# Kernel optimization log

Measured on AMD Instinct MI355X. Metric: run time of the kernel, lower is better.

## Reference

```python
import jax, jax.numpy as jnp
import numpy as np

T, H, F, E, TOP_K = 2048, 1024, 4096, 8, 2


def setup_inputs() -> dict:
    key = jax.random.key(0)
    k0, k1, k2, k3, k4 = jax.random.split(key, 5)
    return {
        "hidden_states": jax.random.normal(k0, (T, H), dtype=jnp.float32),
        "gate_w": jax.random.normal(k1, (E, H), dtype=jnp.float32) * 0.02,  # [E, H] (out, in)
        "w1": jax.random.normal(k2, (E, F, H), dtype=jnp.float32) * 0.02,
        "w2": jax.random.normal(k3, (E, H, F), dtype=jnp.float32) * 0.02,
        "w3": jax.random.normal(k4, (E, F, H), dtype=jnp.float32) * 0.02,
    }


def reference(hidden_states, gate_w, w1, w2, w3):
    # Router: logits -> soft-capped tanh -> fp32 softmax -> top-k
    logits = hidden_states @ gate_w.T                       # [T, E]
    logits = 30.0 * jnp.tanh(logits / 30.0)
    probs = jax.nn.softmax(logits.astype(jnp.float32), axis=-1)
    vals, idx = jax.lax.top_k(probs, TOP_K)                 # [T, K]
    vals = vals.astype(hidden_states.dtype)
    # combine[t, e] = sum_k vals[t, k] * (idx[t, k] == e)
    combine = jnp.sum(
        jax.nn.one_hot(idx, E, dtype=vals.dtype) * vals[..., None], axis=1
    )                                                       # [T, E]
    # Per-expert SwiGLU-style MLP (GELU gate), computed densely and combined
    # with routing weights (zero weight == token not routed to expert).
    g = jax.nn.gelu(jnp.einsum('th,efh->etf', hidden_states, w1), approximate=False)
    u = jnp.einsum('th,efh->etf', hidden_states, w3)        # [E, T, F]
    out = jnp.einsum('etf,ehf->eth', g * u, w2)             # [E, T, H]
    return jnp.einsum('eth,te->th', out, combine)           # [T, H]
```

## Files before the change

### kernel.cpp

```cpp
#include <hip/hip_runtime.h>
#include <hip/hip_bf16.h>

#define TT 2048
#define HH 1024
#define FF 4096
#define NE 8

#define BM1 256
#define BN1 128
#define BM2 128
#define BN2 128
#define BK  32
#define LDK 40

typedef __attribute__((ext_vector_type(4))) float f4;
typedef __attribute__((ext_vector_type(4))) short s4;
typedef __attribute__((ext_vector_type(8))) short s8;

static __device__ __forceinline__ short f2bf(float x) {
  union { __hip_bfloat16 b; short s; } u;
  u.b = __float2bfloat16(x);
  return u.s;
}

__global__ __launch_bounds__(256) void k_router(
    const float* __restrict__ h, const float* __restrict__ gw,
    int* __restrict__ cnt, int* __restrict__ tok, float* __restrict__ wt)
{
  const int lane = threadIdx.x & 63;
  const int wid  = threadIdx.x >> 6;
  const int t = blockIdx.x * 4 + wid;
  const float* hr = h + (size_t)t * HH;

  float acc[NE];
#pragma unroll
  for (int e = 0; e < NE; e++) acc[e] = 0.f;
#pragma unroll 4
  for (int i = 0; i < HH / 64; i++) {
    float hv = hr[lane + (i << 6)];
#pragma unroll
    for (int e = 0; e < NE; e++) acc[e] += hv * gw[e * HH + lane + (i << 6)];
  }
#pragma unroll
  for (int e = 0; e < NE; e++) {
    float v = acc[e];
#pragma unroll
    for (int s = 32; s > 0; s >>= 1) v += __shfl_xor(v, s);
    acc[e] = v;
  }
  if (lane == 0) {
    float p[NE];
    float m = -1e30f;
#pragma unroll
    for (int e = 0; e < NE; e++) {
      p[e] = 30.f * tanhf(acc[e] * (1.f / 30.f));
      m = fmaxf(m, p[e]);
    }
    float s = 0.f;
#pragma unroll
    for (int e = 0; e < NE; e++) { p[e] = expf(p[e] - m); s += p[e]; }
    const float inv = 1.f / s;
    int e1 = 0;
#pragma unroll
    for (int e = 1; e < NE; e++) if (p[e] > p[e1]) e1 = e;
    int e2 = (e1 == 0) ? 1 : 0;
#pragma unroll
    for (int e = 0; e < NE; e++) if (e != e1 && p[e] > p[e2]) e2 = e;

    int pos1 = atomicAdd(&cnt[e1], 1);
    tok[e1 * TT + pos1] = t;
    wt [e1 * TT + pos1] = p[e1] * inv;
    int pos2 = atomicAdd(&cnt[e2], 1);
    tok[e2 * TT + pos2] = t;
    wt [e2 * TT + pos2] = p[e2] * inv;
  }
}

__global__ __launch_bounds__(512) void k_ffn1(
    const float* __restrict__ h, const float* __restrict__ w1,
    const float* __restrict__ w3, const int* __restrict__ cnt,
    const int* __restrict__ tok, __hip_bfloat16* __restrict__ act)
{
  const int e  = blockIdx.z;
  const int mt = blockIdx.y;
  const int nt = blockIdx.x;
  const int ce = cnt[e];
  if (mt * BM1 >= ce) return;
  int base = 0;
  for (int i = 0; i < e; i++) base += cnt[i];

  __shared__ short As [BM1][LDK];
  __shared__ short B1s[BN1][LDK];
  __shared__ short B3s[BN1][LDK];

  const int tid  = threadIdx.x;
  const int lane = tid & 63;
  const int wid  = tid >> 6;
  const int wm   = wid >> 1;
  const int wn   = wid & 1;

  const int ar = tid >> 3;
  const int ac = (tid & 7) << 2;

  const float* ap[4];
#pragma unroll
  for (int p = 0; p < 4; p++) {
    int pos = mt * BM1 + p * 64 + ar;
    int tk = tok[e * TT + ((pos < ce) ? pos : 0)];
    ap[p] = h + (size_t)tk * HH + ac;
  }
  const float* b1p[2];
  const float* b3p[2];
#pragma unroll
  for (int p = 0; p < 2; p++) {
    int fr = nt * BN1 + p * 64 + ar;
    b1p[p] = w1 + ((size_t)e * FF + fr) * HH + ac;
    b3p[p] = w3 + ((size_t)e * FF + fr) * HH + ac;
  }

  f4 accg[4][4], accu[4][4];
#pragma unroll
  for (int i = 0; i < 4; i++)
#pragma unroll
    for (int j = 0; j < 4; j++) {
      f4 z = {0.f, 0.f, 0.f, 0.f};
      accg[i][j] = z; accu[i][j] = z;
    }

  for (int kk = 0; kk < HH; kk += BK) {
#pragma unroll
    for (int p = 0; p < 4; p++) {
      f4 v = *(const f4*)(ap[p] + kk);
      s4 b = { f2bf(v.x), f2bf(v.y), f2bf(v.z), f2bf(v.w) };
      *(s4*)&As[p * 64 + ar][ac] = b;
    }
#pragma unroll
    for (int p = 0; p < 2; p++) {
      f4 v = *(const f4*)(b1p[p] + kk);
      s4 b = { f2bf(v.x), f2bf(v.y), f2bf(v.z), f2bf(v.w) };
      *(s4*)&B1s[p * 64 + ar][ac] = b;
      f4 w = *(const f4*)(b3p[p] + kk);
      s4 c = { f2bf(w.x), f2bf(w.y), f2bf(w.z), f2bf(w.w) };
      *(s4*)&B3s[p * 64 + ar][ac] = c;
    }
    __syncthreads();

    s8 af[4], b1f[4], b3f[4];
    const int fr = lane & 15;
    const int fk = (lane >> 4) << 3;
#pragma unroll
    for (int i = 0; i < 4; i++) {
      af [i] = *(const s8*)&As [wm * 64 + i * 16 + fr][fk];
      b1f[i] = *(const s8*)&B1s[wn * 64 + i * 16 + fr][fk];
      b3f[i] = *(const s8*)&B3s[wn * 64 + i * 16 + fr][fk];
    }
#pragma unroll
    for (int i = 0; i < 4; i++)
#pragma unroll
      for (int j = 0; j < 4; j++) {
        accg[i][j] = __builtin_amdgcn_mfma_f32_16x16x32_bf16(af[i], b1f[j], accg[i][j], 0, 0, 0);
        accu[i][j] = __builtin_amdgcn_mfma_f32_16x16x32_bf16(af[i], b3f[j], accu[i][j], 0, 0, 0);
      }
    __syncthreads();
  }

#pragma unroll
  for (int i = 0; i < 4; i++)
#pragma unroll
    for (int j = 0; j < 4; j++)
#pragma unroll
      for (int r = 0; r < 4; r++) {
        int rr = mt * BM1 + wm * 64 + i * 16 + ((lane >> 4) << 2) + r;
        if (rr < ce) {
          float g = accg[i][j][r];
          float u = accu[i][j][r];
          float a = 0.5f * g * (1.f + erff(g * 0.70710678118f)) * u;
          act[(size_t)(base + rr) * FF + nt * BN1 + wn * 64 + j * 16 + (lane & 15)] =
              __float2bfloat16(a);
        }
      }
}

__global__ __launch_bounds__(256) void k_ffn2(
    const __hip_bfloat16* __restrict__ act, const float* __restrict__ w2,
    const int* __restrict__ cnt, const int* __restrict__ tok,
    const float* __restrict__ wt, float* __restrict__ out)
{
  const int e  = blockIdx.z;
  const int mt = blockIdx.y;
  const int nt = blockIdx.x;
  const int ce = cnt[e];
  if (mt * BM2 >= ce) return;
  int base = 0;
  for (int i = 0; i < e; i++) base += cnt[i];

  __shared__ short As[BM2][LDK];
  __shared__ short Bs[BN2][LDK];

  const int tid  = threadIdx.x;
  const int lane = tid & 63;
  const int wid  = tid >> 6;
  const int wm   = wid >> 1;
  const int wn   = wid & 1;

  const __hip_bfloat16* apt[2];
#pragma unroll
  for (int p = 0; p < 2; p++) {
    int row = mt * BM2 + p * 64 + (tid >> 2);
    int rc = (row < ce) ? row : (ce - 1);
    apt[p] = act + (size_t)(base + rc) * FF + ((tid & 3) << 3);
  }
  const float* bp[4];
#pragma unroll
  for (int p = 0; p < 4; p++) {
    int hr = nt * BN2 + p * 32 + (tid >> 3);
    bp[p] = w2 + ((size_t)e * HH + hr) * FF + ((tid & 7) << 2);
  }

  f4 acc[4][4];
#pragma unroll
  for (int i = 0; i < 4; i++)
#pragma unroll
    for (int j = 0; j < 4; j++) {
      f4 z = {0.f, 0.f, 0.f, 0.f};
      acc[i][j] = z;
    }

  for (int kk = 0; kk < FF; kk += BK) {
#pragma unroll
    for (int p = 0; p < 2; p++) {
      s8 v = *(const s8*)(apt[p] + kk);
      *(s8*)&As[p * 64 + (tid >> 2)][(tid & 3) << 3] = v;
    }
#pragma unroll
    for (int p = 0; p < 4; p++) {
      f4 v = *(const f4*)(bp[p] + kk);
      s4 b = { f2bf(v.x), f2bf(v.y), f2bf(v.z), f2bf(v.w) };
      *(s4*)&Bs[p * 32 + (tid >> 3)][(tid & 7) << 2] = b;
    }
    __syncthreads();

    s8 af[4], bfr[4];
    const int fr = lane & 15;
    const int fk = (lane >> 4) << 3;
#pragma unroll
    for (int i = 0; i < 4; i++) {
      af [i] = *(const s8*)&As[wm * 64 + i * 16 + fr][fk];
      bfr[i] = *(const s8*)&Bs[wn * 64 + i * 16 + fr][fk];
    }
#pragma unroll
    for (int i = 0; i < 4; i++)
#pragma unroll
      for (int j = 0; j < 4; j++)
        acc[i][j] = __builtin_amdgcn_mfma_f32_16x16x32_bf16(af[i], bfr[j], acc[i][j], 0, 0, 0);
    __syncthreads();
  }

#pragma unroll
  for (int i = 0; i < 4; i++)
#pragma unroll
    for (int j = 0; j < 4; j++)
#pragma unroll
      for (int r = 0; r < 4; r++) {
        int rr = mt * BM2 + wm * 64 + i * 16 + ((lane >> 4) << 2) + r;
        if (rr < ce) {
          int   tkn = tok[e * TT + rr];
          float w   = wt [e * TT + rr];
          atomicAdd(&out[(size_t)tkn * HH + nt * BN2 + wn * 64 + j * 16 + (lane & 15)],
                    acc[i][j][r] * w);
        }
      }
}

extern "C" void kernel_launch(void* const* d_in, const int* in_sizes, int n_in,
                              void* d_out, int out_size, void* d_ws, size_t ws_size,
                              hipStream_t stream)
{
  (void)in_sizes; (void)n_in; (void)ws_size;
  const float* h  = (const float*)d_in[0];
  const float* gw = (const float*)d_in[1];
  const float* w1 = (const float*)d_in[2];
  const float* w2 = (const float*)d_in[3];
  const float* w3 = (const float*)d_in[4];
  float* out = (float*)d_out;

  char* ws = (char*)d_ws;
  int*   cnt = (int*)ws;
  int*   tok = (int*)(ws + 1024);
  float* wtp = (float*)(ws + 1024 + 65536);
  __hip_bfloat16* act = (__hip_bfloat16*)(ws + 262144);

  hipMemsetAsync(cnt, 0, 32, stream);
  hipMemsetAsync(d_out, 0, (size_t)out_size * sizeof(float), stream);

  k_router<<<dim3(TT / 4), dim3(256), 0, stream>>>(h, gw, cnt, tok, wtp);
  k_ffn1<<<dim3(FF / BN1, 8, NE), dim3(512), 0, stream>>>(h, w1, w3, cnt, tok, act);
  k_ffn2<<<dim3(HH / BN2, 16, NE), dim3(256), 0, stream>>>(act, w2, cnt, tok, wtp, out);
}
```

Before: 728.2 us.

## Pre-convert weights to bf16, use direct global-to-LDS loads, split-K FFN2

Adds conversion kernels that turn the activations and all three weight tensors into bf16 buffers in workspace before the GEMMs run. FFN1 is split into two passes: the first computes the up projection into act, and the second computes the gate projection and applies GELU times up on the fly. Both GEMMs now stage tiles with global_load_lds 16-byte loads at BK=64, and FFN2 splits K four ways with atomic accumulation. This costs an extra full pass over roughly 400MB of fp32 weights every call, re-reads hidden states, and adds more atomics, in exchange for simpler and faster inner loops. The LDS layout is unpadded, so bank conflicts are possible.

```diff
diff --git a/kernel.cpp b/kernel.cpp
--- a/kernel.cpp
+++ b/kernel.cpp
@@ -5,13 +5,7 @@
 #define HH 1024
 #define FF 4096
 #define NE 8
-
-#define BM1 256
-#define BN1 128
-#define BM2 128
-#define BN2 128
-#define BK  32
-#define LDK 40
+#define BK 64
 
 typedef __attribute__((ext_vector_type(4))) float f4;
 typedef __attribute__((ext_vector_type(4))) short s4;
@@ -21,6 +15,26 @@
   union { __hip_bfloat16 b; short s; } u;
   u.b = __float2bfloat16(x);
   return u.s;
+}
+
+static __device__ __forceinline__ void gload16(const void* g, void* l) {
+  __builtin_amdgcn_global_load_lds(
+      (const __attribute__((address_space(1))) void*)g,
+      (__attribute__((address_space(3))) void*)l, 16, 0, 0);
+}
+
+__global__ __launch_bounds__(256) void k_cvt(
+    const float* __restrict__ src, __hip_bfloat16* __restrict__ dst, int n8)
+{
+  int i = blockIdx.x * blockDim.x + threadIdx.x;
+  const int stride = gridDim.x * blockDim.x;
+  for (; i < n8; i += stride) {
+    f4 a = ((const f4*)src)[2 * i];
+    f4 b = ((const f4*)src)[2 * i + 1];
+    s8 o = { f2bf(a.x), f2bf(a.y), f2bf(a.z), f2bf(a.w),
+             f2bf(b.x), f2bf(b.y), f2bf(b.z), f2bf(b.w) };
+    ((s8*)dst)[i] = o;
+  }
 }
 
 __global__ __launch_bounds__(256) void k_router(
@@ -76,22 +90,22 @@
   }
 }
 
-__global__ __launch_bounds__(512) void k_ffn1(
-    const float* __restrict__ h, const float* __restrict__ w1,
-    const float* __restrict__ w3, const int* __restrict__ cnt,
-    const int* __restrict__ tok, __hip_bfloat16* __restrict__ act)
+template<bool GPASS>
+__global__ __launch_bounds__(256) void k_ffn1(
+    const __hip_bfloat16* __restrict__ hb, const __hip_bfloat16* __restrict__ wb,
+    const int* __restrict__ cnt, const int* __restrict__ tok,
+    __hip_bfloat16* __restrict__ act)
 {
   const int e  = blockIdx.z;
   const int mt = blockIdx.y;
   const int nt = blockIdx.x;
   const int ce = cnt[e];
-  if (mt * BM1 >= ce) return;
+  if (mt * 128 >= ce) return;
   int base = 0;
   for (int i = 0; i < e; i++) base += cnt[i];
 
-  __shared__ short As [BM1][LDK];
-  __shared__ short B1s[BN1][LDK];
-  __shared__ short B3s[BN1][LDK];
+  __shared__ short As[128 * BK];
+  __shared__ short Bs[128 * BK];
 
   const int tid  = threadIdx.x;
   const int lane = tid & 63;
@@ -99,103 +113,92 @@
   const int wm   = wid >> 1;
   const int wn   = wid & 1;
 
-  const int ar = tid >> 3;
-  const int ac = (tid & 7) << 2;
-
-  const float* ap[4];
-#pragma unroll
-  for (int p = 0; p < 4; p++) {
-    int pos = mt * BM1 + p * 64 + ar;
-    int tk = tok[e * TT + ((pos < ce) ? pos : 0)];
-    ap[p] = h + (size_t)tk * HH + ac;
-  }
-  const float* b1p[2];
-  const float* b3p[2];
-#pragma unroll
-  for (int p = 0; p < 2; p++) {
-    int fr = nt * BN1 + p * 64 + ar;
-    b1p[p] = w1 + ((size_t)e * FF + fr) * HH + ac;
-    b3p[p] = w3 + ((size_t)e * FF + fr) * HH + ac;
-  }
-
-  f4 accg[4][4], accu[4][4];
+  const int srow = (wid << 3) + (lane >> 3);
+  const int scol = (lane & 7) << 3;
+  const __hip_bfloat16* asrc[4];
+#pragma unroll
+  for (int i = 0; i < 4; i++) {
+    int pos = mt * 128 + i * 32 + srow;
+    int tk  = tok[e * TT + min(pos, ce - 1)];
+    asrc[i] = hb + (size_t)tk * HH + scol;
+  }
+  const __hip_bfloat16* bsrc[4];
+#pragma unroll
+  for (int i = 0; i < 4; i++) {
+    int fr = nt * 128 + i * 32 + srow;
+    bsrc[i] = wb + ((size_t)e * FF + fr) * HH + scol;
+  }
+
+  f4 acc[4][4];
 #pragma unroll
   for (int i = 0; i < 4; i++)
 #pragma unroll
-    for (int j = 0; j < 4; j++) {
-      f4 z = {0.f, 0.f, 0.f, 0.f};
-      accg[i][j] = z; accu[i][j] = z;
-    }
+    for (int j = 0; j < 4; j++) { f4 z = {0.f,0.f,0.f,0.f}; acc[i][j] = z; }
 
   for (int kk = 0; kk < HH; kk += BK) {
 #pragma unroll
-    for (int p = 0; p < 4; p++) {
-      f4 v = *(const f4*)(ap[p] + kk);
-      s4 b = { f2bf(v.x), f2bf(v.y), f2bf(v.z), f2bf(v.w) };
-      *(s4*)&As[p * 64 + ar][ac] = b;
-    }
-#pragma unroll
-    for (int p = 0; p < 2; p++) {
-      f4 v = *(const f4*)(b1p[p] + kk);
-      s4 b = { f2bf(v.x), f2bf(v.y), f2bf(v.z), f2bf(v.w) };
-      *(s4*)&B1s[p * 64 + ar][ac] = b;
-      f4 w = *(const f4*)(b3p[p] + kk);
-      s4 c = { f2bf(w.x), f2bf(w.y), f2bf(w.z), f2bf(w.w) };
-      *(s4*)&B3s[p * 64 + ar][ac] = c;
+    for (int i = 0; i < 4; i++) {
+      gload16(asrc[i] + kk, &As[(i * 32 + (wid << 3)) * BK]);
+      gload16(bsrc[i] + kk, &Bs[(i * 32 + (wid << 3)) * BK]);
     }
     __syncthreads();
-
-    s8 af[4], b1f[4], b3f[4];
-    const int fr = lane & 15;
-    const int fk = (lane >> 4) << 3;
-#pragma unroll
-    for (int i = 0; i < 4; i++) {
-      af [i] = *(const s8*)&As [wm * 64 + i * 16 + fr][fk];
-      b1f[i] = *(const s8*)&B1s[wn * 64 + i * 16 + fr][fk];
-      b3f[i] = *(const s8*)&B3s[wn * 64 + i * 16 + fr][fk];
-    }
-#pragma unroll
-    for (int i = 0; i < 4; i++)
-#pragma unroll
-      for (int j = 0; j < 4; j++) {
-        accg[i][j] = __builtin_amdgcn_mfma_f32_16x16x32_bf16(af[i], b1f[j], accg[i][j], 0, 0, 0);
-        accu[i][j] = __builtin_amdgcn_mfma_f32_16x16x32_bf16(af[i], b3f[j], accu[i][j], 0, 0, 0);
-      }
+#pragma unroll
+    for (int ks = 0; ks < 2; ks++) {
+      const int ko = ks * 32 + ((lane >> 4) << 3);
+      s8 af[4], bf_[4];
+#pragma unroll
+      for (int i = 0; i < 4; i++)
+        af[i]  = *(const s8*)&As[(wm * 64 + i * 16 + (lane & 15)) * BK + ko];
+#pragma unroll
+      for (int j = 0; j < 4; j++)
+        bf_[j] = *(const s8*)&Bs[(wn * 64 + j * 16 + (lane & 15)) * BK + ko];
+#pragma unroll
+      for (int i = 0; i < 4; i++)
+#pragma unroll
+        for (int j = 0; j < 4; j++)
+          acc[i][j] = __builtin_amdgcn_mfma_f32_16x16x32_bf16(af[i], bf_[j], acc[i][j], 0, 0, 0);
+    }
     __syncthreads();
   }
 
+  const int orow0 = wm * 64 + ((lane >> 4) << 2);
+  const int ocol0 = nt * 128 + wn * 64 + (lane & 15);
 #pragma unroll
   for (int i = 0; i < 4; i++)
 #pragma unroll
-    for (int j = 0; j < 4; j++)
-#pragma unroll
-      for (int r = 0; r < 4; r++) {
-        int rr = mt * BM1 + wm * 64 + i * 16 + ((lane >> 4) << 2) + r;
-        if (rr < ce) {
-          float g = accg[i][j][r];
-          float u = accu[i][j][r];
-          float a = 0.5f * g * (1.f + erff(g * 0.70710678118f)) * u;
-          act[(size_t)(base + rr) * FF + nt * BN1 + wn * 64 + j * 16 + (lane & 15)] =
-              __float2bfloat16(a);
+    for (int r = 0; r < 4; r++) {
+      int rr = mt * 128 + orow0 + i * 16 + r;
+      if (rr < ce) {
+        size_t rowoff = (size_t)(base + rr) * FF + ocol0;
+#pragma unroll
+        for (int j = 0; j < 4; j++) {
+          float v = acc[i][j][r];
+          if (GPASS) {
+            float u = __bfloat162float(act[rowoff + j * 16]);
+            v = 0.5f * v * (1.f + erff(v * 0.70710678118f)) * u;
+          }
+          act[rowoff + j * 16] = __float2bfloat16(v);
         }
       }
+    }
 }
 
 __global__ __launch_bounds__(256) void k_ffn2(
-    const __hip_bfloat16* __restrict__ act, const float* __restrict__ w2,
+    const __hip_bfloat16* __restrict__ act, const __hip_bfloat16* __restrict__ w2b,
     const int* __restrict__ cnt, const int* __restrict__ tok,
     const float* __restrict__ wt, float* __restrict__ out)
 {
-  const int e  = blockIdx.z;
+  const int e  = blockIdx.z >> 2;
+  const int sk = blockIdx.z & 3;
   const int mt = blockIdx.y;
   const int nt = blockIdx.x;
   const int ce = cnt[e];
-  if (mt * BM2 >= ce) return;
+  if (mt * 128 >= ce) return;
   int base = 0;
   for (int i = 0; i < e; i++) base += cnt[i];
 
-  __shared__ short As[BM2][LDK];
-  __shared__ short Bs[BN2][LDK];
+  __shared__ short As[128 * BK];
+  __shared__ short Bs[128 * BK];
 
   const int tid  = threadIdx.x;
   const int lane = tid & 63;
@@ -203,73 +206,70 @@
   const int wm   = wid >> 1;
   const int wn   = wid & 1;
 
-  const __hip_bfloat16* apt[2];
-#pragma unroll
-  for (int p = 0; p < 2; p++) {
-    int row = mt * BM2 + p * 64 + (tid >> 2);
-    int rc = (row < ce) ? row : (ce - 1);
-    apt[p] = act + (size_t)(base + rc) * FF + ((tid & 3) << 3);
-  }
-  const float* bp[4];
-#pragma unroll
-  for (int p = 0; p < 4; p++) {
-    int hr = nt * BN2 + p * 32 + (tid >> 3);
-    bp[p] = w2 + ((size_t)e * HH + hr) * FF + ((tid & 7) << 2);
+  const int srow = (wid << 3) + (lane >> 3);
+  const int scol = (lane & 7) << 3;
+  const __hip_bfloat16* asrc[4];
+#pragma unroll
+  for (int i = 0; i < 4; i++) {
+    int pos = mt * 128 + i * 32 + srow;
+    int rc  = min(pos, ce - 1);
+    asrc[i] = act + (size_t)(base + rc) * FF + (sk << 10) + scol;
+  }
+  const __hip_bfloat16* bsrc[4];
+#pragma unroll
+  for (int i = 0; i < 4; i++) {
+    int hr = nt * 128 + i * 32 + srow;
+    bsrc[i] = w2b + ((size_t)e * HH + hr) * FF + (sk << 10) + scol;
   }
 
   f4 acc[4][4];
 #pragma unroll
   for (int i = 0; i < 4; i++)
 #pragma unroll
-    for (int j = 0; j < 4; j++) {
-      f4 z = {0.f, 0.f, 0.f, 0.f};
-      acc[i][j] = z;
-    }
-
-  for (int kk = 0; kk < FF; kk += BK) {
-#pragma unroll
-    for (int p = 0; p < 2; p++) {
-      s8 v = *(const s8*)(apt[p] + kk);
-      *(s8*)&As[p * 64 + (tid >> 2)][(tid & 3) << 3] = v;
-    }
-#pragma unroll
-    for (int p = 0; p < 4; p++) {
-      f4 v = *(const f4*)(bp[p] + kk);
-      s4 b = { f2bf(v.x), f2bf(v.y), f2bf(v.z), f2bf(v.w) };
-      *(s4*)&Bs[p * 32 + (tid >> 3)][(tid & 7) << 2] = b;
+    for (int j = 0; j < 4; j++) { f4 z = {0.f,0.f,0.f,0.f}; acc[i][j] = z; }
+
+  for (int kk = 0; kk < 1024; kk += BK) {
+#pragma unroll
+    for (int i = 0; i < 4; i++) {
+      gload16(asrc[i] + kk, &As[(i * 32 + (wid << 3)) * BK]);
+      gload16(bsrc[i] + kk, &Bs[(i * 32 + (wid << 3)) * BK]);
     }
     __syncthreads();
-
-    s8 af[4], bfr[4];
-    const int fr = lane & 15;
-    const int fk = (lane >> 4) << 3;
-#pragma unroll
-    for (int i = 0; i < 4; i++) {
-      af [i] = *(const s8*)&As[wm * 64 + i * 16 + fr][fk];
-      bfr[i] = *(const s8*)&Bs[wn * 64 + i * 16 + fr][fk];
-    }
-#pragma unroll
-    for (int i = 0; i < 4; i++)
+#pragma unroll
+    for (int ks = 0; ks < 2; ks++) {
+      const int ko = ks * 32 + ((lane >> 4) << 3);
+      s8 af[4], bf_[4];
+#pragma unroll
+      for (int i = 0; i < 4; i++)
+        af[i]  = *(const s8*)&As[(wm * 64 + i * 16 + (lane & 15)) * BK + ko];
 #pragma unroll
       for (int j = 0; j < 4; j++)
-        acc[i][j] = __builtin_amdgcn_mfma_f32_16x16x32_bf16(af[i], bfr[j], acc[i][j], 0, 0, 0);
+        bf_[j] = *(const s8*)&Bs[(wn * 64 + j * 16 + (lane & 15)) * BK + ko];
+#pragma unroll
+      for (int i = 0; i < 4; i++)
+#pragma unroll
+        for (int j = 0; j < 4; j++)
+          acc[i][j] = __builtin_amdgcn_mfma_f32_16x16x32_bf16(af[i], bf_[j], acc[i][j], 0, 0, 0);
+    }
     __syncthreads();
   }
 
+  const int orow0 = wm * 64 + ((lane >> 4) << 2);
+  const int ocol0 = nt * 128 + wn * 64 + (lane & 15);
 #pragma unroll
   for (int i = 0; i < 4; i++)
 #pragma unroll
-    for (int j = 0; j < 4; j++)
-#pragma unroll
-      for (int r = 0; r < 4; r++) {
-        int rr = mt * BM2 + wm * 64 + i * 16 + ((lane >> 4) << 2) + r;
-        if (rr < ce) {
-          int   tkn = tok[e * TT + rr];
-          float w   = wt [e * TT + rr];
-          atomicAdd(&out[(size_t)tkn * HH + nt * BN2 + wn * 64 + j * 16 + (lane & 15)],
-                    acc[i][j][r] * w);
-        }
+    for (int r = 0; r < 4; r++) {
+      int rr = mt * 128 + orow0 + i * 16 + r;
+      if (rr < ce) {
+        int   tkn = tok[e * TT + rr];
+        float w   = wt [e * TT + rr];
+        float* orow = out + (size_t)tkn * HH + ocol0;
+#pragma unroll
+        for (int j = 0; j < 4; j++)
+          atomicAdd(&orow[j * 16], acc[i][j][r] * w);
       }
+    }
 }
 
 extern "C" void kernel_launch(void* const* d_in, const int* in_sizes, int n_in,
@@ -289,11 +289,22 @@
   int*   tok = (int*)(ws + 1024);
   float* wtp = (float*)(ws + 1024 + 65536);
   __hip_bfloat16* act = (__hip_bfloat16*)(ws + 262144);
+  __hip_bfloat16* hb  = (__hip_bfloat16*)(ws + 262144 + 33554432);
+  __hip_bfloat16* w1b = hb  + (size_t)TT * HH;
+  __hip_bfloat16* w3b = w1b + (size_t)NE * FF * HH;
+  __hip_bfloat16* w2b = w3b + (size_t)NE * FF * HH;
 
   hipMemsetAsync(cnt, 0, 32, stream);
   hipMemsetAsync(d_out, 0, (size_t)out_size * sizeof(float), stream);
 
+  k_cvt<<<dim3(1024), dim3(256), 0, stream>>>(h,  hb,  TT * HH / 8);
+  k_cvt<<<dim3(2048), dim3(256), 0, stream>>>(w1, w1b, NE * FF * HH / 8);
+  k_cvt<<<dim3(2048), dim3(256), 0, stream>>>(w3, w3b, NE * FF * HH / 8);
+  k_cvt<<<dim3(2048), dim3(256), 0, stream>>>(w2, w2b, NE * HH * FF / 8);
+
   k_router<<<dim3(TT / 4), dim3(256), 0, stream>>>(h, gw, cnt, tok, wtp);
-  k_ffn1<<<dim3(FF / BN1, 8, NE), dim3(512), 0, stream>>>(h, w1, w3, cnt, tok, act);
-  k_ffn2<<<dim3(HH / BN2, 16, NE), dim3(256), 0, stream>>>(act, w2, cnt, tok, wtp, out);
-}
+
+  k_ffn1<false><<<dim3(FF / 128, 16, NE), dim3(256), 0, stream>>>(hb, w3b, cnt, tok, act);
+  k_ffn1<true ><<<dim3(FF / 128, 16, NE), dim3(256), 0, stream>>>(hb, w1b, cnt, tok, act);
+  k_ffn2<<<dim3(HH / 128, 16, NE * 4), dim3(256), 0, stream>>>(act, w2b, cnt, tok, wtp, out);
+}
```

After: 743.0 us. +2.0%, slower.
